# Optimization experiments

Hardware: AMD Instinct MI355X
Metric: run time of the kernel (lower is better)

Reference implementation:

```python
import jax, jax.numpy as jnp
import numpy as np

N_NODES = 100000
N_EDGES = 3200000
F_IN = 16
HID = 64
K = 4
N_LAYERS = 3
SLOPE = 0.01  # LeakyReLU default negative slope


def _gcn_norm(src, dst, edge_weight, n):
    # PyG gcn_norm with add_self_loops=False: deg over targets
    deg = jax.ops.segment_sum(edge_weight, dst, num_segments=n)
    dinv = jnp.where(deg > 0, jax.lax.rsqrt(jnp.maximum(deg, 1e-30)), 0.0)
    return dinv[src] * edge_weight * dinv[dst]


def _tag_conv(x, src, dst, norm, Ws, b):
    # out = sum_{k=0..K} (A_norm^k x) @ Ws[k] + b ; Ws: [K+1, in, out]
    out = x @ Ws[0]
    h = x
    for k in range(1, Ws.shape[0]):
        msg = norm[:, None] * h[src]                      # [E, in]
        h = jax.ops.segment_sum(msg, dst, num_segments=x.shape[0])
        out = out + h @ Ws[k]
    return out + b


def leaky_relu(x):
    return jnp.where(x >= 0, x, SLOPE * x)


def setup_inputs() -> dict:
    key = jax.random.key(0)
    ks = jax.random.split(key, 10)
    x = jax.random.normal(ks[0], (N_NODES, F_IN), dtype=jnp.float32)
    edge_index = jax.random.randint(ks[1], (2, N_EDGES), 0, N_NODES, dtype=jnp.int64)
    edge_weight = jax.random.uniform(ks[2], (N_EDGES,), dtype=jnp.float32)
    batch = jnp.zeros((N_NODES,), dtype=jnp.int64)
    s1 = 1.0 / np.sqrt(F_IN)
    s2 = 1.0 / np.sqrt(HID)
    W1 = jax.random.uniform(ks[3], (K + 1, F_IN, HID), jnp.float32, -s1, s1)
    b1 = jnp.zeros((HID,), jnp.float32)
    W2 = jax.random.uniform(ks[4], (N_LAYERS - 1, K + 1, HID, HID), jnp.float32, -s2, s2)
    b2 = jnp.zeros((N_LAYERS - 1, HID), jnp.float32)
    Wout = jax.random.uniform(ks[5], (HID, 1), jnp.float32, -s2, s2)
    bout = jnp.zeros((1,), jnp.float32)
    return {"x": x, "edge_index": edge_index, "edge_weight": edge_weight,
            "batch": batch, "W1": W1, "b1": b1, "W2": W2, "b2": b2,
            "Wout": Wout, "bout": bout}


def reference(x, edge_index, edge_weight, batch, W1, b1, W2, b2, Wout, bout):
    src, dst = edge_index[0], edge_index[1]
    norm = _gcn_norm(src, dst, edge_weight, x.shape[0])
    h = _tag_conv(x, src, dst, norm, W1, b1)
    h = leaky_relu(h)  # dropout p=0 -> identity (inference)
    for i in range(N_LAYERS - 1):
        h = _tag_conv(h, src, dst, norm, W2[i], b2[i])
        h = leaky_relu(h)
    # reghead_layers == 1 -> singleLinear
    return h @ Wout + bout
```

## Files before the change

kernel.cpp:

```cpp
#include <hip/hip_runtime.h>
#include <hip/hip_cooperative_groups.h>

namespace cg = cooperative_groups;


typedef unsigned long long u64;
typedef unsigned int u32;

__device__ __forceinline__ float h2f(unsigned short u) {
  _Float16 h;
  __builtin_memcpy(&h, &u, 2);
  return (float)h;
}
__device__ __forceinline__ unsigned short f2h(float f) {
  _Float16 h = (_Float16)f;
  unsigned short u;
  __builtin_memcpy(&u, &h, 2);
  return u;
}
__device__ __forceinline__ ushort4 pack_h(float4 v) {
  ushort4 r;
  r.x = f2h(v.x); r.y = f2h(v.y); r.z = f2h(v.z); r.w = f2h(v.w);
  return r;
}
__device__ __forceinline__ float4 unpack_h(ushort4 u) {
  return make_float4(h2f(u.x), h2f(u.y), h2f(u.z), h2f(u.w));
}
__device__ __forceinline__ void dec_ep(u32 u, int& s, float& w) {
  s = (int)(u & 0x1FFFFu);
  w = h2f((unsigned short)(u >> 17));
}


__global__ __launch_bounds__(256) void k_hist(const int* __restrict__ dst, u32* __restrict__ H,
                                              int E, int CH, int NB,
                                              const float4* __restrict__ x4,
                                              ushort4* __restrict__ xh, int n4) {
  __shared__ u32 hc[1024];
  int tid = threadIdx.x, blk = blockIdx.x, nblk = gridDim.x;
  for (int i = tid; i < 1024; i += 256) hc[i] = 0;
  for (int i = blk * 256 + tid; i < n4; i += nblk * 256) xh[i] = pack_h(x4[i]);
  __syncthreads();
  int e0 = blk * CH, e1 = min(E, e0 + CH);
  for (int e = e0 + tid; e < e1; e += 256) atomicAdd(&hc[((u32)dst[e]) >> 7], 1u);
  __syncthreads();
  for (int c = tid; c < NB; c += 256) H[(size_t)c * nblk + blk] = hc[c];
}

__global__ void scanH_blocks(u32* __restrict__ H, u32* __restrict__ bsum, int n) {
  __shared__ u32 s[256];
  int tid = threadIdx.x;
  int i = blockIdx.x * 256 + tid;
  u32 v = (i < n) ? H[i] : 0;
  s[tid] = v;
  __syncthreads();
#pragma unroll
  for (int off = 1; off < 256; off <<= 1) {
    u32 t = (tid >= off) ? s[tid - off] : 0;
    __syncthreads();
    s[tid] += t;
    __syncthreads();
  }
  if (i < n) H[i] = s[tid] - v;
  if (tid == 255) bsum[blockIdx.x] = s[255];
}

__global__ void scanH_sums(u32* __restrict__ bsum, int nb) {
  __shared__ u32 s[1024];
  int tid = threadIdx.x;
  u32 v = (tid < nb) ? bsum[tid] : 0;
  s[tid] = v;
  __syncthreads();
#pragma unroll
  for (int off = 1; off < 1024; off <<= 1) {
    u32 t = (tid >= off) ? s[tid - off] : 0;
    __syncthreads();
    s[tid] += t;
    __syncthreads();
  }
  if (tid < nb) bsum[tid] = s[tid] - v;
}

__global__ void scanH_add(u32* __restrict__ H, const u32* __restrict__ bsum, int n) {
  int i = blockIdx.x * blockDim.x + threadIdx.x;
  if (i < n) H[i] += bsum[i >> 8];
}

__global__ __launch_bounds__(256) void k_scatter(const int* __restrict__ src,
                                                 const int* __restrict__ dst,
                                                 const float* __restrict__ w,
                                                 const u32* __restrict__ H,
                                                 u64* __restrict__ sorted, int E, int CH, int NB) {
  __shared__ u32 cur[1024];
  int tid = threadIdx.x, blk = blockIdx.x, nblk = gridDim.x;
  for (int c = tid; c < NB; c += 256) cur[c] = H[(size_t)c * nblk + blk];
  __syncthreads();
  int e0 = blk * CH, e1 = min(E, e0 + CH);
  for (int e = e0 + tid; e < e1; e += 256) {
    int d = dst[e];
    int c = ((u32)d) >> 7;
    u32 p = atomicAdd(&cur[c], 1u);
    u64 it = (u64)(u32)src[e] | ((u64)((u32)d & 127u) << 17) |
             ((u64)__float_as_uint(w[e]) << 24);
    sorted[p] = it;
  }
}

#define BCAP 6144
__global__ __launch_bounds__(256) void k_bucket(u64* __restrict__ sorted,
                                                const u32* __restrict__ H, int NBLK,
                                                int* __restrict__ ptr, float* __restrict__ dinv,
                                                int N, int E, int NB) {
  __shared__ u64 stage[BCAP];
  __shared__ u32 cnt[128], base[128], cur[128], tmp[128];
  __shared__ float ws[128];
  int c = blockIdx.x, tid = threadIdx.x;
  int b0 = (int)H[(size_t)c * NBLK];
  int b1 = (c + 1 < NB) ? (int)H[(size_t)(c + 1) * NBLK] : E;
  int m = b1 - b0;
  if (tid < 128) { cnt[tid] = 0; ws[tid] = 0.f; }
  __syncthreads();
  for (int i = tid; i < m; i += 256) {
    u64 it = sorted[b0 + i];
    stage[i] = it;
    int lo = (int)((it >> 17) & 127u);
    atomicAdd(&cnt[lo], 1u);
    atomicAdd(&ws[lo], __uint_as_float((u32)(it >> 24)));
  }
  __syncthreads();
  u32 v = (tid < 128) ? cnt[tid] : 0;
  if (tid < 128) tmp[tid] = v;
  __syncthreads();
#pragma unroll
  for (int off = 1; off < 128; off <<= 1) {
    u32 t = 0;
    if (tid < 128 && tid >= off) t = tmp[tid - off];
    __syncthreads();
    if (tid < 128) tmp[tid] += t;
    __syncthreads();
  }
  if (tid < 128) {
    base[tid] = tmp[tid] - v;
    cur[tid] = tmp[tid] - v;
    int node = c * 128 + tid;
    if (node < N) {
      ptr[node] = b0 + (int)base[tid];
      float d = ws[tid];
      dinv[node] = (d > 0.f) ? rsqrtf(fmaxf(d, 1e-30f)) : 0.f;
    }
  }
  if (c == NB - 1 && tid == 0) ptr[N] = E;
  __syncthreads();
  for (int i = tid; i < m; i += 256) {
    u64 it = stage[i];
    int lo = (int)((it >> 17) & 127u);
    u32 p = atomicAdd(&cur[lo], 1u);
    sorted[b0 + (int)p] = it;
  }
}

__global__ __launch_bounds__(256) void k_pack(const u64* __restrict__ sorted,
                                              const float* __restrict__ dinv,
                                              const u32* __restrict__ H, int NBLK,
                                              u32* __restrict__ ep, int E, int NB) {
  int c = blockIdx.x;
  int b0 = (int)H[(size_t)c * NBLK];
  int b1 = (c + 1 < NB) ? (int)H[(size_t)(c + 1) * NBLK] : E;
  for (int i = b0 + threadIdx.x; i < b1; i += 256) {
    u64 it = sorted[i];
    int s = (int)(it & 0x1FFFFu);
    int dn = c * 128 + (int)((it >> 17) & 127u);
    float wv = __uint_as_float((u32)(it >> 24));
    float nv = dinv[s] * wv * dinv[dn];
    ep[i] = ((u32)f2h(nv) << 17) | (u32)s;
  }
}

__device__ __forceinline__ void acc_e(float4& a, u32 pe, ushort4 h) {
  float w = h2f((unsigned short)(pe >> 17));
  a.x = fmaf(w, h2f(h.x), a.x); a.y = fmaf(w, h2f(h.y), a.y);
  a.z = fmaf(w, h2f(h.z), a.z); a.w = fmaf(w, h2f(h.w), a.w);
}

template <int F4>
__device__ __forceinline__ float4 gather(const int* __restrict__ ptr, const u32* __restrict__ ep,
                                         const ushort4* __restrict__ hin, int node, int f4) {
  int e0 = ptr[node], e1 = ptr[node + 1];
  float4 a = make_float4(0.f, 0.f, 0.f, 0.f);
  int e = e0;
  while (e < e1 && (e & 3)) {
    u32 pe = ep[e];
    acc_e(a, pe, hin[(size_t)(pe & 0x1FFFFu) * F4 + f4]);
    ++e;
  }
  int nq = (e1 - e) >> 2;
  if (nq > 0) {
    uint4 p = *(const uint4*)(ep + e);
    ushort4 h0 = hin[(size_t)(p.x & 0x1FFFFu) * F4 + f4];
    ushort4 h1 = hin[(size_t)(p.y & 0x1FFFFu) * F4 + f4];
    ushort4 h2 = hin[(size_t)(p.z & 0x1FFFFu) * F4 + f4];
    ushort4 h3 = hin[(size_t)(p.w & 0x1FFFFu) * F4 + f4];
    for (int q = 1; q < nq; ++q) {
      uint4 pn = *(const uint4*)(ep + e + 4 * q);
      ushort4 g0 = hin[(size_t)(pn.x & 0x1FFFFu) * F4 + f4];
      ushort4 g1 = hin[(size_t)(pn.y & 0x1FFFFu) * F4 + f4];
      ushort4 g2 = hin[(size_t)(pn.z & 0x1FFFFu) * F4 + f4];
      ushort4 g3 = hin[(size_t)(pn.w & 0x1FFFFu) * F4 + f4];
      acc_e(a, p.x, h0); acc_e(a, p.y, h1);
      acc_e(a, p.z, h2); acc_e(a, p.w, h3);
      p = pn; h0 = g0; h1 = g1; h2 = g2; h3 = g3;
    }
    acc_e(a, p.x, h0); acc_e(a, p.y, h1);
    acc_e(a, p.z, h2); acc_e(a, p.w, h3);
    e += nq * 4;
  }
  while (e < e1) {
    u32 pe = ep[e];
    acc_e(a, pe, hin[(size_t)(pe & 0x1FFFFu) * F4 + f4]);
    ++e;
  }
  return a;
}

__device__ __forceinline__ void mm_acc(const float* __restrict__ tl, const float4* __restrict__ Wl,
                                       int ln, int j4, float4& a) {
#pragma unroll 8
  for (int i = 0; i < 64; ++i) {
    float tv = tl[ln * 64 + ((((i >> 2) ^ ln) << 2) | (i & 3))];
    float4 wv = Wl[i * 16 + j4];
    a.x = fmaf(tv, wv.x, a.x); a.y = fmaf(tv, wv.y, a.y);
    a.z = fmaf(tv, wv.z, a.z); a.w = fmaf(tv, wv.w, a.w);
  }
}

template <int NC>
__global__ __launch_bounds__(256) void mega_k(
    const int* __restrict__ ptr, const u32* __restrict__ ep,
    ushort4* __restrict__ hb0, ushort4* __restrict__ hb1, ushort4* __restrict__ hb2,
    const float* __restrict__ W2, const float* __restrict__ b2,
    const float* __restrict__ Wout, const float* __restrict__ bout,
    float* __restrict__ outv, int n) {
  cg::grid_group grid = cg::this_grid();
  __shared__ float4 Wl[1024];
  __shared__ float4 tl4[256];
  const float* tl = (const float*)tl4;
  const int tid = threadIdx.x, j4 = tid & 15, ln = tid >> 4;
  const int nb = (int)gridDim.x;
  float4 acc[NC];

  for (int L = 0; L < 2; ++L) {
    const float* WL = W2 + (size_t)L * 5 * 4096;
#pragma unroll
    for (int c = 0; c < NC; ++c) acc[c] = make_float4(0.f, 0.f, 0.f, 0.f);

    {
      const float4* W04 = (const float4*)WL;
      for (int i = tid; i < 1024; i += 256) Wl[i] = W04[i];
      __syncthreads();
#pragma unroll
      for (int c = 0; c < NC; ++c) {
        int node = (c * nb + (int)blockIdx.x) * 16 + ln;
        float4 own = make_float4(0.f, 0.f, 0.f, 0.f);
        if (node < n) own = unpack_h(hb2[(size_t)node * 16 + j4]);
        tl4[ln * 16 + (j4 ^ ln)] = own;
        mm_acc(tl, Wl, ln, j4, acc[c]);
      }
      __syncthreads();
    }

    for (int k = 1; k <= 4; ++k) {
      const ushort4* gsrc = (k == 1) ? hb2 : ((k == 3) ? hb1 : hb0);
      ushort4* gdst = (k == 2) ? hb1 : hb0;
      const bool last = (k == 4);
      const float4* Wk4 = (const float4*)(WL + (size_t)k * 4096);
      for (int i = tid; i < 1024; i += 256) Wl[i] = Wk4[i];
      __syncthreads();
#pragma unroll
      for (int c = 0; c < NC; ++c) {
        int node = (c * nb + (int)blockIdx.x) * 16 + ln;
        float4 t = make_float4(0.f, 0.f, 0.f, 0.f);
        if (node < n) {
          t = gather<16>(ptr, ep, gsrc, node, j4);
          if (!last) gdst[(size_t)node * 16 + j4] = pack_h(t);
        }
        tl4[ln * 16 + (j4 ^ ln)] = t;
        mm_acc(tl, Wl, ln, j4, acc[c]);
      }
      if (last) {
        const float4* bias4 = (const float4*)(b2 + (size_t)L * 64);
#pragma unroll
        for (int c = 0; c < NC; ++c) {
          int node = (c * nb + (int)blockIdx.x) * 16 + ln;
          if (node >= n) continue;
          float4 a = acc[c];
          float4 b = bias4[j4];
          a.x += b.x; a.y += b.y; a.z += b.z; a.w += b.w;
          a.x = (a.x >= 0.f) ? a.x : 0.01f * a.x;
          a.y = (a.y >= 0.f) ? a.y : 0.01f * a.y;
          a.z = (a.z >= 0.f) ? a.z : 0.01f * a.z;
          a.w = (a.w >= 0.f) ? a.w : 0.01f * a.w;
          if (L == 0) {
            hb2[(size_t)node * 16 + j4] = pack_h(a);
          } else {
            float v = a.x * Wout[4 * j4] + a.y * Wout[4 * j4 + 1] +
                      a.z * Wout[4 * j4 + 2] + a.w * Wout[4 * j4 + 3];
            v += __shfl_down(v, 8, 16);
            v += __shfl_down(v, 4, 16);
            v += __shfl_down(v, 2, 16);
            v += __shfl_down(v, 1, 16);
            if (j4 == 0) outv[node] = v + bout[0];
          }
        }
      }
      if (!(L == 1 && k == 4)) {
        __threadfence();
        grid.sync();
      }
    }
  }
}

template <bool FIRST, bool LAST, bool HEAD>
__launch_bounds__(256)
__global__ void ptag64_k(const int* __restrict__ ptr, const u32* __restrict__ ep,
                         const ushort4* __restrict__ hin, ushort4* __restrict__ hout,
                         const float4* __restrict__ Wk4, const float4* __restrict__ W04,
                         ushort4* __restrict__ acch, const float4* __restrict__ bias4,
                         const float* __restrict__ Wout, const float* __restrict__ bout,
                         float* __restrict__ outv, int n) {
  __shared__ float4 Wl[1024];
  __shared__ float4 tl4[256];
  const float* tl = (const float*)tl4;
  int tid = threadIdx.x;
  for (int i = tid; i < 1024; i += 256) Wl[i] = Wk4[i];
  int gid = blockIdx.x * 256 + tid;
  int node = gid >> 4, j4 = gid & 15, ln = tid >> 4;

  float4 t = make_float4(0.f, 0.f, 0.f, 0.f);
  if (node < n) {
    t = gather<16>(ptr, ep, hin, node, j4);
    if (!LAST) hout[(size_t)node * 16 + j4] = pack_h(t);
  }
  tl4[ln * 16 + (j4 ^ ln)] = t;
  __syncthreads();

  float4 a = make_float4(0.f, 0.f, 0.f, 0.f);
  if (!FIRST && node < n) a = unpack_h(acch[(size_t)node * 16 + j4]);
  mm_acc(tl, Wl, ln, j4, a);
  if (FIRST) {
    __syncthreads();
    for (int i = tid; i < 1024; i += 256) Wl[i] = W04[i];
    float4 own = make_float4(0.f, 0.f, 0.f, 0.f);
    if (node < n) own = unpack_h(hin[(size_t)node * 16 + j4]);
    tl4[ln * 16 + (j4 ^ ln)] = own;
    __syncthreads();
    mm_acc(tl, Wl, ln, j4, a);
  }
  if (node >= n) return;

  if (LAST) {
    float4 b = bias4[j4];
    a.x += b.x; a.y += b.y; a.z += b.z; a.w += b.w;
    a.x = (a.x >= 0.f) ? a.x : 0.01f * a.x;
    a.y = (a.y >= 0.f) ? a.y : 0.01f * a.y;
    a.z = (a.z >= 0.f) ? a.z : 0.01f * a.z;
    a.w = (a.w >= 0.f) ? a.w : 0.01f * a.w;
    if (HEAD) {
      float v = a.x * Wout[4 * j4] + a.y * Wout[4 * j4 + 1] +
                a.z * Wout[4 * j4 + 2] + a.w * Wout[4 * j4 + 3];
      v += __shfl_down(v, 8, 16);
      v += __shfl_down(v, 4, 16);
      v += __shfl_down(v, 2, 16);
      v += __shfl_down(v, 1, 16);
      if (j4 == 0) outv[node] = v + bout[0];
    } else {
      hout[(size_t)node * 16 + j4] = pack_h(a);
    }
  } else {
    acch[(size_t)node * 16 + j4] = pack_h(a);
  }
}

template <bool FIRST, bool LAST>
__launch_bounds__(256)
__global__ void ptag16_k(const int* __restrict__ ptr, const u32* __restrict__ ep,
                         const ushort4* __restrict__ hin, ushort4* __restrict__ hout,
                         const float4* __restrict__ Wk4, const float4* __restrict__ W04,
                         ushort4* __restrict__ acch, const float4* __restrict__ bias4,
                         ushort4* __restrict__ outbuf, int n) {
  __shared__ float4 Wl[256];
  __shared__ float4 W0l[FIRST ? 256 : 1];
  __shared__ float4 tl4[64 * 5];
  const float* tl = (const float*)tl4;
  int tid = threadIdx.x;
  Wl[tid] = Wk4[tid];
  if (FIRST) W0l[tid] = W04[tid];
  int gid = blockIdx.x * 256 + tid;
  int node = gid >> 2, q = tid & 3, ln = tid >> 2;

  float4 t = make_float4(0.f, 0.f, 0.f, 0.f);
  if (node < n) {
    t = gather<4>(ptr, ep, hin, node, q);
    if (!LAST) hout[(size_t)node * 4 + q] = pack_h(t);
  }
  tl4[ln * 5 + q] = t;
  __syncthreads();

  float4 a[4];
#pragma unroll
  for (int c = 0; c < 4; ++c) a[c] = make_float4(0.f, 0.f, 0.f, 0.f);
  if (!FIRST && node < n) {
#pragma unroll
    for (int c = 0; c < 4; ++c) a[c] = unpack_h(acch[(size_t)node * 16 + 4 * q + c]);
  }
#pragma unroll 4
  for (int i = 0; i < 16; ++i) {
    float tv = tl[ln * 20 + i];
#pragma unroll
    for (int c = 0; c < 4; ++c) {
      float4 wv = Wl[i * 16 + 4 * q + c];
      a[c].x = fmaf(tv, wv.x, a[c].x); a[c].y = fmaf(tv, wv.y, a[c].y);
      a[c].z = fmaf(tv, wv.z, a[c].z); a[c].w = fmaf(tv, wv.w, a[c].w);
    }
  }
  if (FIRST) {
    __syncthreads();
    float4 own = make_float4(0.f, 0.f, 0.f, 0.f);
    if (node < n) own = unpack_h(hin[(size_t)node * 4 + q]);
    tl4[ln * 5 + q] = own;
    __syncthreads();
#pragma unroll 4
    for (int i = 0; i < 16; ++i) {
      float tv = tl[ln * 20 + i];
#pragma unroll
      for (int c = 0; c < 4; ++c) {
        float4 wv = W0l[i * 16 + 4 * q + c];
        a[c].x = fmaf(tv, wv.x, a[c].x); a[c].y = fmaf(tv, wv.y, a[c].y);
        a[c].z = fmaf(tv, wv.z, a[c].z); a[c].w = fmaf(tv, wv.w, a[c].w);
      }
    }
  }
  if (node >= n) return;

  if (LAST) {
#pragma unroll
    for (int c = 0; c < 4; ++c) {
      float4 b = bias4[4 * q + c];
      a[c].x += b.x; a[c].y += b.y; a[c].z += b.z; a[c].w += b.w;
      a[c].x = (a[c].x >= 0.f) ? a[c].x : 0.01f * a[c].x;
      a[c].y = (a[c].y >= 0.f) ? a[c].y : 0.01f * a[c].y;
      a[c].z = (a[c].z >= 0.f) ? a[c].z : 0.01f * a[c].z;
      a[c].w = (a[c].w >= 0.f) ? a[c].w : 0.01f * a[c].w;
      outbuf[(size_t)node * 16 + 4 * q + c] = pack_h(a[c]);
    }
  } else {
#pragma unroll
    for (int c = 0; c < 4; ++c) acch[(size_t)node * 16 + 4 * q + c] = pack_h(a[c]);
  }
}

extern "C" void kernel_launch(void* const* d_in, const int* in_sizes, int n_in,
                              void* d_out, int out_size, void* d_ws, size_t ws_size,
                              hipStream_t stream) {
  const float* x    = (const float*)d_in[0];
  const int*   ei   = (const int*)d_in[1];
  const float* ew   = (const float*)d_in[2];
  const float* W1   = (const float*)d_in[4];
  const float* b1   = (const float*)d_in[5];
  const float* W2   = (const float*)d_in[6];
  const float* b2   = (const float*)d_in[7];
  const float* Wout = (const float*)d_in[8];
  const float* bout = (const float*)d_in[9];
  float* out = (float*)d_out;

  const int N = in_sizes[0] / 16;
  const int E = in_sizes[2];
  const int* src = ei;
  const int* dst = ei + E;

  const int NBLK = 256;
  const int CH = (E + NBLK - 1) / NBLK;
  const int NB = (N + 127) >> 7;
  const int HN = NB * NBLK;

  char* ws = (char*)d_ws;
  size_t off = 0;
  auto alloc = [&](size_t bytes) {
    char* p = ws + off;
    off = (off + bytes + 255) & ~(size_t)255;
    return p;
  };
  u32*     H      = (u32*)alloc((size_t)HN * 4);
  u32*     bsum   = (u32*)alloc(4096);
  float*   dinv   = (float*)alloc((size_t)N * 4);
  int*     ptr    = (int*)alloc(((size_t)N + 1) * 4);
  u64*     sorted = (u64*)alloc((size_t)E * 8);
  u32*     ep     = (u32*)alloc((size_t)E * 4);
  ushort4* xh     = (ushort4*)alloc((size_t)N * 16 * 2);
  ushort4* hb0    = (ushort4*)alloc((size_t)N * 64 * 2);
  ushort4* hb1    = (ushort4*)alloc((size_t)N * 64 * 2);
  ushort4* hb2    = (ushort4*)alloc((size_t)N * 64 * 2);
  ushort4* acch   = (ushort4*)alloc((size_t)N * 64 * 2);

  k_hist<<<NBLK, 256, 0, stream>>>(dst, H, E, CH, NB, (const float4*)x, xh, N * 4);
  scanH_blocks<<<HN / 256, 256, 0, stream>>>(H, bsum, HN);
  scanH_sums<<<1, 1024, 0, stream>>>(bsum, HN / 256);
  scanH_add<<<HN / 256, 256, 0, stream>>>(H, bsum, HN);
  k_scatter<<<NBLK, 256, 0, stream>>>(src, dst, ew, H, sorted, E, CH, NB);
  k_bucket<<<NB, 256, 0, stream>>>(sorted, H, NBLK, ptr, dinv, N, E, NB);
  k_pack<<<NB, 256, 0, stream>>>(sorted, dinv, H, NBLK, ep, E, NB);

  int g4  = (N * 4 + 255) / 256;
  int g16 = (N * 16 + 255) / 256;

  auto W1k = [&](int k) { return (const float4*)(W1 + (size_t)k * 1024); };
  auto W2k = [&](int l, int k) { return (const float4*)(W2 + ((size_t)l * 5 + k) * 4096); };

  ptag16_k<true,  false><<<g4, 256, 0, stream>>>(ptr, ep, xh,  hb0, W1k(1), W1k(0), acch, nullptr, nullptr, N);
  ptag16_k<false, false><<<g4, 256, 0, stream>>>(ptr, ep, hb0, hb1, W1k(2), nullptr, acch, nullptr, nullptr, N);
  ptag16_k<false, false><<<g4, 256, 0, stream>>>(ptr, ep, hb1, hb0, W1k(3), nullptr, acch, nullptr, nullptr, N);
  ptag16_k<false, true ><<<g4, 256, 0, stream>>>(ptr, ep, hb0, nullptr, W1k(4), nullptr, acch,
                                                 (const float4*)b1, hb2, N);

  int maxB4 = 0, maxB5 = 0, maxB7 = 0;
  (void)hipOccupancyMaxActiveBlocksPerMultiprocessor(&maxB4, mega_k<4>, 256, 0);
  (void)hipOccupancyMaxActiveBlocksPerMultiprocessor(&maxB5, mega_k<5>, 256, 0);
  (void)hipOccupancyMaxActiveBlocksPerMultiprocessor(&maxB7, mega_k<7>, 256, 0);
  void* fn = nullptr;
  int grid = 0;
  if ((long)maxB4 * 256 * 16 * 4 >= (long)N) {
    fn = (void*)mega_k<4>; grid = maxB4 * 256;
  } else if ((long)maxB5 * 256 * 16 * 5 >= (long)N) {
    fn = (void*)mega_k<5>; grid = maxB5 * 256;
  } else if ((long)maxB7 * 256 * 16 * 7 >= (long)N) {
    fn = (void*)mega_k<7>; grid = maxB7 * 256;
  }

  if (fn) {
    const int* ptrA = ptr; const u32* epA = ep;
    ushort4 *h0A = hb0, *h1A = hb1, *h2A = hb2;
    const float *W2A = W2, *b2A = b2, *WoA = Wout, *boA = bout;
    float* outA = out; int nA = N;
    void* args[] = {&ptrA, &epA, &h0A, &h1A, &h2A, &W2A, &b2A, &WoA, &boA, &outA, &nA};
    hipLaunchCooperativeKernel(fn, dim3(grid), dim3(256), args, 0, stream);
  } else {
    ptag64_k<true,  false, false><<<g16, 256, 0, stream>>>(ptr, ep, hb2, hb0, W2k(0,1), W2k(0,0), acch,
                                                           nullptr, nullptr, nullptr, nullptr, N);
    ptag64_k<false, false, false><<<g16, 256, 0, stream>>>(ptr, ep, hb0, hb1, W2k(0,2), nullptr, acch,
                                                           nullptr, nullptr, nullptr, nullptr, N);
    ptag64_k<false, false, false><<<g16, 256, 0, stream>>>(ptr, ep, hb1, hb0, W2k(0,3), nullptr, acch,
                                                           nullptr, nullptr, nullptr, nullptr, N);
    ptag64_k<false, true,  false><<<g16, 256, 0, stream>>>(ptr, ep, hb0, hb2, W2k(0,4), nullptr, acch,
                                                           (const float4*)b2, nullptr, nullptr, nullptr, N);
    ptag64_k<true,  false, false><<<g16, 256, 0, stream>>>(ptr, ep, hb2, hb0, W2k(1,1), W2k(1,0), acch,
                                                           nullptr, nullptr, nullptr, nullptr, N);
    ptag64_k<false, false, false><<<g16, 256, 0, stream>>>(ptr, ep, hb0, hb1, W2k(1,2), nullptr, acch,
                                                           nullptr, nullptr, nullptr, nullptr, N);
    ptag64_k<false, false, false><<<g16, 256, 0, stream>>>(ptr, ep, hb1, hb0, W2k(1,3), nullptr, acch,
                                                           nullptr, nullptr, nullptr, nullptr, N);
    ptag64_k<false, true,  true ><<<g16, 256, 0, stream>>>(ptr, ep, hb0, nullptr, W2k(1,4), nullptr, acch,
                                                           (const float4*)(b2 + 64), Wout, bout, out, N);
  }
}
```

Measured before the change: 1.001 ms.

## Gather 16-byte feature chunks with edge-split lanes and shuffle reduction

After: 953.6 us. -4.7%, faster.

```diff
diff --git a/kernel.cpp b/kernel.cpp
--- a/kernel.cpp
+++ b/kernel.cpp
@@ -190,22 +190,22 @@
   int e = e0;
   while (e < e1 && (e & 3)) {
     u32 pe = ep[e];
-    acc_e(a, pe, hin[(size_t)(pe & 0x1FFFFu) * F4 + f4]);
+    acc_e(a, pe, hin[(u32)(pe & 0x1FFFFu) * F4 + f4]);
     ++e;
   }
   int nq = (e1 - e) >> 2;
   if (nq > 0) {
     uint4 p = *(const uint4*)(ep + e);
-    ushort4 h0 = hin[(size_t)(p.x & 0x1FFFFu) * F4 + f4];
-    ushort4 h1 = hin[(size_t)(p.y & 0x1FFFFu) * F4 + f4];
-    ushort4 h2 = hin[(size_t)(p.z & 0x1FFFFu) * F4 + f4];
-    ushort4 h3 = hin[(size_t)(p.w & 0x1FFFFu) * F4 + f4];
+    ushort4 h0 = hin[(u32)(p.x & 0x1FFFFu) * F4 + f4];
+    ushort4 h1 = hin[(u32)(p.y & 0x1FFFFu) * F4 + f4];
+    ushort4 h2 = hin[(u32)(p.z & 0x1FFFFu) * F4 + f4];
+    ushort4 h3 = hin[(u32)(p.w & 0x1FFFFu) * F4 + f4];
     for (int q = 1; q < nq; ++q) {
       uint4 pn = *(const uint4*)(ep + e + 4 * q);
-      ushort4 g0 = hin[(size_t)(pn.x & 0x1FFFFu) * F4 + f4];
-      ushort4 g1 = hin[(size_t)(pn.y & 0x1FFFFu) * F4 + f4];
-      ushort4 g2 = hin[(size_t)(pn.z & 0x1FFFFu) * F4 + f4];
-      ushort4 g3 = hin[(size_t)(pn.w & 0x1FFFFu) * F4 + f4];
+      ushort4 g0 = hin[(u32)(pn.x & 0x1FFFFu) * F4 + f4];
+      ushort4 g1 = hin[(u32)(pn.y & 0x1FFFFu) * F4 + f4];
+      ushort4 g2 = hin[(u32)(pn.z & 0x1FFFFu) * F4 + f4];
+      ushort4 g3 = hin[(u32)(pn.w & 0x1FFFFu) * F4 + f4];
       acc_e(a, p.x, h0); acc_e(a, p.y, h1);
       acc_e(a, p.z, h2); acc_e(a, p.w, h3);
       p = pn; h0 = g0; h1 = g1; h2 = g2; h3 = g3;
@@ -216,10 +216,72 @@
   }
   while (e < e1) {
     u32 pe = ep[e];
-    acc_e(a, pe, hin[(size_t)(pe & 0x1FFFFu) * F4 + f4]);
+    acc_e(a, pe, hin[(u32)(pe & 0x1FFFFu) * F4 + f4]);
     ++e;
   }
   return a;
+}
+
+__device__ __forceinline__ void acc8(float4& a0, float4& a1, u32 pe, uint4 r) {
+  float w = h2f((unsigned short)(pe >> 17));
+  a0.x = fmaf(w, h2f((unsigned short)(r.x & 0xFFFFu)), a0.x);
+  a0.y = fmaf(w, h2f((unsigned short)(r.x >> 16)), a0.y);
+  a0.z = fmaf(w, h2f((unsigned short)(r.y & 0xFFFFu)), a0.z);
+  a0.w = fmaf(w, h2f((unsigned short)(r.y >> 16)), a0.w);
+  a1.x = fmaf(w, h2f((unsigned short)(r.z & 0xFFFFu)), a1.x);
+  a1.y = fmaf(w, h2f((unsigned short)(r.z >> 16)), a1.y);
+  a1.z = fmaf(w, h2f((unsigned short)(r.w & 0xFFFFu)), a1.z);
+  a1.w = fmaf(w, h2f((unsigned short)(r.w >> 16)), a1.w);
+}
+
+__device__ __forceinline__ void gather64o(const int* __restrict__ ptr, const u32* __restrict__ ep,
+                                          const ushort4* __restrict__ hin, int node,
+                                          int f8, int o, float4& a0, float4& a1) {
+  int e0 = ptr[node], e1 = ptr[node + 1];
+  const u32 foff = 2u * (u32)f8;
+  int e = e0;
+  while (e < e1 && (e & 3)) {
+    if ((e & 1) == o) {
+      u32 pe = ep[e];
+      uint4 r = *(const uint4*)(hin + ((u32)(pe & 0x1FFFFu) * 16u + foff));
+      acc8(a0, a1, pe, r);
+    }
+    ++e;
+  }
+  int nq = (e1 - e) >> 2;
+  int q = o;
+  if (q < nq) {
+    uint4 p = *(const uint4*)(ep + e + 4 * q);
+    uint4 r0 = *(const uint4*)(hin + ((u32)(p.x & 0x1FFFFu) * 16u + foff));
+    uint4 r1 = *(const uint4*)(hin + ((u32)(p.y & 0x1FFFFu) * 16u + foff));
+    for (;;) {
+      uint4 r2 = *(const uint4*)(hin + ((u32)(p.z & 0x1FFFFu) * 16u + foff));
+      uint4 r3 = *(const uint4*)(hin + ((u32)(p.w & 0x1FFFFu) * 16u + foff));
+      acc8(a0, a1, p.x, r0);
+      acc8(a0, a1, p.y, r1);
+      int qn = q + 2;
+      if (qn >= nq) {
+        acc8(a0, a1, p.z, r2);
+        acc8(a0, a1, p.w, r3);
+        break;
+      }
+      uint4 pn = *(const uint4*)(ep + e + 4 * qn);
+      r0 = *(const uint4*)(hin + ((u32)(pn.x & 0x1FFFFu) * 16u + foff));
+      r1 = *(const uint4*)(hin + ((u32)(pn.y & 0x1FFFFu) * 16u + foff));
+      acc8(a0, a1, p.z, r2);
+      acc8(a0, a1, p.w, r3);
+      p = pn; q = qn;
+    }
+  }
+  e += nq * 4;
+  while (e < e1) {
+    if ((e & 1) == o) {
+      u32 pe = ep[e];
+      uint4 r = *(const uint4*)(hin + ((u32)(pe & 0x1FFFFu) * 16u + foff));
+      acc8(a0, a1, pe, r);
+    }
+    ++e;
+  }
 }
 
 __device__ __forceinline__ void mm_acc(const float* __restrict__ tl, const float4* __restrict__ Wl,
@@ -335,13 +397,19 @@
   for (int i = tid; i < 1024; i += 256) Wl[i] = Wk4[i];
   int gid = blockIdx.x * 256 + tid;
   int node = gid >> 4, j4 = gid & 15, ln = tid >> 4;
-
-  float4 t = make_float4(0.f, 0.f, 0.f, 0.f);
-  if (node < n) {
-    t = gather<16>(ptr, ep, hin, node, j4);
-    if (!LAST) hout[(size_t)node * 16 + j4] = pack_h(t);
-  }
-  tl4[ln * 16 + (j4 ^ ln)] = t;
+  const int o = j4 >> 3, f8 = j4 & 7;
+
+  float4 a0 = make_float4(0.f, 0.f, 0.f, 0.f);
+  float4 a1 = make_float4(0.f, 0.f, 0.f, 0.f);
+  if (node < n) gather64o(ptr, ep, hin, node, f8, o, a0, a1);
+  a0.x += __shfl_xor(a0.x, 8, 16); a0.y += __shfl_xor(a0.y, 8, 16);
+  a0.z += __shfl_xor(a0.z, 8, 16); a0.w += __shfl_xor(a0.w, 8, 16);
+  a1.x += __shfl_xor(a1.x, 8, 16); a1.y += __shfl_xor(a1.y, 8, 16);
+  a1.z += __shfl_xor(a1.z, 8, 16); a1.w += __shfl_xor(a1.w, 8, 16);
+  float4 t = (o == 0) ? a0 : a1;
+  int g = 2 * f8 + o;
+  if (node < n && !LAST) hout[(size_t)node * 16 + g] = pack_h(t);
+  tl4[ln * 16 + (g ^ ln)] = t;
   __syncthreads();
 
   float4 a = make_float4(0.f, 0.f, 0.f, 0.f);
```
